# Kernel optimization log

Measured on AMD Instinct MI355X. Metric: run time of the kernel, lower is better.

## Reference

```python
import jax, jax.numpy as jnp
import numpy as np

N_NODES = 100000
N_EDGES = 600000
HIDDEN = 128


def setup_inputs() -> dict:
    key = jax.random.key(0)
    k_x, k_s, k_r, k_ws, k_wm = jax.random.split(key, 5)
    scale = 1.0 / np.sqrt(HIDDEN)
    return {
        "x": jax.random.normal(k_x, (N_NODES, HIDDEN), dtype=jnp.float32),
        "senders": jax.random.randint(k_s, (N_EDGES,), 0, N_NODES, dtype=jnp.int32),
        "receivers": jax.random.randint(k_r, (N_EDGES,), 0, N_NODES, dtype=jnp.int32),
        "weight_self": jax.random.normal(k_ws, (HIDDEN, HIDDEN), dtype=jnp.float32) * scale,
        "weight_msg": jax.random.normal(k_wm, (HIDDEN, HIDDEN), dtype=jnp.float32) * scale,
        "bias": jnp.zeros((HIDDEN,), dtype=jnp.float32),
    }


def reference(x, senders, receivers, weight_self, weight_msg, bias):
    n_nodes = x.shape[0]
    # gather messages along edges: (E, H)
    messages = x[senders]
    # scatter-add aggregate at receivers: (N, H)
    agg = jnp.zeros_like(x).at[receivers].add(messages)
    # in-degree count, clamped to >= 1
    degree = jnp.zeros((n_nodes,), dtype=x.dtype).at[receivers].add(1.0)
    degree = jnp.maximum(degree, 1.0)[:, None]
    msg_mean = agg / degree
    out = x @ weight_self + msg_mean @ weight_msg + bias
    return jax.nn.relu(out)
```

## Files before the change

kernel.cpp:

```cpp
#include <hip/hip_runtime.h>

#define N_NODES 100000
#define N_EDGES 600000
#define H 128
#define CAP 32

#define NB_FILL 586
#define NB_PREP 16
#define NB_CONV4 3125
#define NB_TOTAL (NB_FILL * 6 + (NB_PREP + NB_CONV4 - NB_FILL * 5))

#define BLK_NODES 64
#define N_BLKS ((N_NODES + BLK_NODES - 1) / BLK_NODES)

typedef short v8s __attribute__((ext_vector_type(8)));
typedef float v4f __attribute__((ext_vector_type(4)));

__device__ __forceinline__ unsigned short f2bf(float f) {
    unsigned int u = __float_as_uint(f);
    u = (u + 0x7fffu + ((u >> 16) & 1u)) >> 16;
    return (unsigned short)u;
}
__device__ __forceinline__ unsigned int pack2bf(float a, float b) {
    return (unsigned int)f2bf(a) | ((unsigned int)f2bf(b) << 16);
}
__device__ __forceinline__ void accum8(float* a, uint4 u) {
    a[0] += __uint_as_float(u.x << 16);
    a[1] += __uint_as_float(u.x & 0xffff0000u);
    a[2] += __uint_as_float(u.y << 16);
    a[3] += __uint_as_float(u.y & 0xffff0000u);
    a[4] += __uint_as_float(u.z << 16);
    a[5] += __uint_as_float(u.z & 0xffff0000u);
    a[6] += __uint_as_float(u.w << 16);
    a[7] += __uint_as_float(u.w & 0xffff0000u);
}

__global__ __launch_bounds__(256) void prep_fused_kernel(
    const float* __restrict__ x, unsigned int* __restrict__ xb4,
    const float* __restrict__ Ws, const float* __restrict__ Wm,
    unsigned short* __restrict__ Bperm,
    const int* __restrict__ senders, const int* __restrict__ receivers,
    int* __restrict__ cnt, int* __restrict__ slots)
{
    int b = blockIdx.x;
    bool isfill = (b % 6 == 0) && (b / 6 < NB_FILL);
    if (isfill) {
        int e = (b / 6) * 1024 + threadIdx.x;
#pragma unroll
        for (int k = 0; k < 4; ++k, e += 256) {
            if (e < N_EDGES) {
                int r = receivers[e];
                int s = senders[e];
                int pos = atomicAdd(&cnt[r], 1);
                if (pos < CAP) __builtin_nontemporal_store(s, &slots[r * CAP + pos]);
            }
        }
    } else {
        int o = (b < NB_FILL * 6) ? (b - b / 6 - 1) : (b - NB_FILL);
        if (o < NB_PREP) {
            int t = o * 256 + threadIdx.x;
            int kstep = t >> 9;
            int ntile = (t >> 6) & 7;
            int lane  = t & 63;
            int q = lane >> 4;
            int n = ntile * 16 + (lane & 15);
#pragma unroll
            for (int j = 0; j < 8; ++j) {
                int k = kstep * 32 + q * 8 + j;
                float v = (k < H) ? Ws[k * H + n] : Wm[(k - H) * H + n];
                Bperm[(size_t)t * 8 + j] = f2bf(v);
            }
        } else {
            int base = (o - NB_PREP) * 1024 + threadIdx.x;
#pragma unroll
            for (int k = 0; k < 4; ++k) {
                int i = base + k * 256;
                float4 v = ((const float4*)x)[i];
                uint2 ov;
                ov.x = pack2bf(v.x, v.y);
                ov.y = pack2bf(v.z, v.w);
                ((uint2*)xb4)[i] = ov;
            }
        }
    }
}

__global__ __launch_bounds__(256) void gather_gemm_kernel(
    const unsigned short* __restrict__ xb,
    const int* __restrict__ cnt,
    const int* __restrict__ slots,
    const unsigned short* __restrict__ Bperm,
    const float* __restrict__ bias,
    float* __restrict__ out)
{
    __shared__ unsigned short tile[2][16][65][8];

    const int t = threadIdx.x;
    const int w = t >> 6;
    const int lane = t & 63;
    const int node_base = blockIdx.x * BLK_NODES;
    const int sub = (lane >> 4) & 3;
    const int li  = lane & 15;

    for (int g = 0; g < 4; ++g) {
        int nl = w * 16 + g * 4 + sub;
        int node = node_base + nl;
        float a[8];
#pragma unroll
        for (int i = 0; i < 8; ++i) a[i] = 0.f;
        int d_true = 0;
        uint4 xcopy = make_uint4(0, 0, 0, 0);
        if (node < N_NODES) {
            xcopy = *(const uint4*)(xb + (size_t)node * H + li * 8);
            d_true = cnt[node];
            int d = d_true < CAP ? d_true : CAP;
            const int* sl = slots + node * CAP;
            int e = 0;
            for (; e + 3 < d; e += 4) {
                int i0 = sl[e];
                int i1 = sl[e + 1];
                int i2 = sl[e + 2];
                int i3 = sl[e + 3];
                uint4 u0 = *(const uint4*)(xb + (size_t)i0 * H + li * 8);
                uint4 u1 = *(const uint4*)(xb + (size_t)i1 * H + li * 8);
                uint4 u2 = *(const uint4*)(xb + (size_t)i2 * H + li * 8);
                uint4 u3 = *(const uint4*)(xb + (size_t)i3 * H + li * 8);
                accum8(a, u0);
                accum8(a, u1);
                accum8(a, u2);
                accum8(a, u3);
            }
            for (; e < d; ++e) {
                uint4 u0 = *(const uint4*)(xb + (size_t)sl[e] * H + li * 8);
                accum8(a, u0);
            }
        }
        float inv = 1.0f / fmaxf((float)d_true, 1.0f);
        uint4 o;
        o.x = pack2bf(a[0] * inv, a[1] * inv);
        o.y = pack2bf(a[2] * inv, a[3] * inv);
        o.z = pack2bf(a[4] * inv, a[5] * inv);
        o.w = pack2bf(a[6] * inv, a[7] * inv);
        *(uint4*)&tile[0][li][nl][0] = xcopy;
        *(uint4*)&tile[1][li][nl][0] = o;
    }
    __syncthreads();

    const int q  = lane >> 4;
    const int mr = lane & 15;

    v4f acc[4][2];
#pragma unroll
    for (int j = 0; j < 2; ++j) {
        float bv = bias[(2 * w + j) * 16 + mr];
#pragma unroll
        for (int s = 0; s < 4; ++s) acc[s][j] = (v4f){bv, bv, bv, bv};
    }

    const v8s* bp = (const v8s*)Bperm;
#pragma unroll
    for (int ks = 0; ks < 8; ++ks) {
        int buf = ks >> 2;
        int lic = (ks & 3) * 4 + q;
        v8s a[4];
#pragma unroll
        for (int s = 0; s < 4; ++s)
            a[s] = *(const v8s*)&tile[buf][lic][s * 16 + mr][0];
#pragma unroll
        for (int j = 0; j < 2; ++j) {
            v8s bfrag = bp[(ks * 8 + 2 * w + j) * 64 + lane];
#pragma unroll
            for (int s = 0; s < 4; ++s)
                acc[s][j] = __builtin_amdgcn_mfma_f32_16x16x32_bf16(a[s], bfrag, acc[s][j], 0, 0, 0);
        }
    }

#pragma unroll
    for (int s = 0; s < 4; ++s) {
#pragma unroll
        for (int r = 0; r < 4; ++r) {
            int row = node_base + s * 16 + q * 4 + r;
            if (row < N_NODES) {
#pragma unroll
                for (int j = 0; j < 2; ++j)
                    out[(size_t)row * H + (2 * w + j) * 16 + mr] = fmaxf(acc[s][j][r], 0.f);
            }
        }
    }
}

extern "C" void kernel_launch(void* const* d_in, const int* in_sizes, int n_in,
                              void* d_out, int out_size, void* d_ws, size_t ws_size,
                              hipStream_t stream) {
    const float* x        = (const float*)d_in[0];
    const int*   senders  = (const int*)d_in[1];
    const int*   receivers= (const int*)d_in[2];
    const float* Ws       = (const float*)d_in[3];
    const float* Wm       = (const float*)d_in[4];
    const float* bias     = (const float*)d_in[5];
    float*       out      = (float*)d_out;

    char* p = (char*)d_ws;
    unsigned short* xb    = (unsigned short*)p; p += (size_t)N_NODES * H * sizeof(unsigned short);
    unsigned short* Bperm = (unsigned short*)p; p += (size_t)256 * H * sizeof(unsigned short);
    int* cnt   = (int*)p; p += (size_t)N_NODES * sizeof(int);
    int* slots = (int*)p; p += (size_t)N_NODES * CAP * sizeof(int);

    hipMemsetAsync(cnt, 0, (size_t)N_NODES * sizeof(int), stream);

    prep_fused_kernel<<<NB_TOTAL, 256, 0, stream>>>(
        x, (unsigned int*)xb, Ws, Wm, Bperm, senders, receivers, cnt, slots);
    gather_gemm_kernel<<<N_BLKS, 256, 0, stream>>>(xb, cnt, slots, Bperm, bias, out);
}
```

Baseline: 186.2 us.

## Use 512-thread gather-GEMM blocks and vectorize edge and slot index loads

Result: faster. 178.3 us (-4.2%).

```diff
diff --git a/kernel.cpp b/kernel.cpp
--- a/kernel.cpp
+++ b/kernel.cpp
@@ -45,15 +45,18 @@
     int b = blockIdx.x;
     bool isfill = (b % 6 == 0) && (b / 6 < NB_FILL);
     if (isfill) {
-        int e = (b / 6) * 1024 + threadIdx.x;
-#pragma unroll
-        for (int k = 0; k < 4; ++k, e += 256) {
-            if (e < N_EDGES) {
-                int r = receivers[e];
-                int s = senders[e];
-                int pos = atomicAdd(&cnt[r], 1);
-                if (pos < CAP) __builtin_nontemporal_store(s, &slots[r * CAP + pos]);
-            }
+        int tid = (b / 6) * 256 + threadIdx.x;
+        if (tid < N_EDGES / 4) {
+            int4 r4 = ((const int4*)receivers)[tid];
+            int4 s4 = ((const int4*)senders)[tid];
+            int p0 = atomicAdd(&cnt[r4.x], 1);
+            int p1 = atomicAdd(&cnt[r4.y], 1);
+            int p2 = atomicAdd(&cnt[r4.z], 1);
+            int p3 = atomicAdd(&cnt[r4.w], 1);
+            if (p0 < CAP) __builtin_nontemporal_store(s4.x, &slots[r4.x * CAP + p0]);
+            if (p1 < CAP) __builtin_nontemporal_store(s4.y, &slots[r4.y * CAP + p1]);
+            if (p2 < CAP) __builtin_nontemporal_store(s4.z, &slots[r4.z * CAP + p2]);
+            if (p3 < CAP) __builtin_nontemporal_store(s4.w, &slots[r4.w * CAP + p3]);
         }
     } else {
         int o = (b < NB_FILL * 6) ? (b - b / 6 - 1) : (b - NB_FILL);
@@ -85,7 +88,7 @@
     }
 }
 
-__global__ __launch_bounds__(256) void gather_gemm_kernel(
+__global__ __launch_bounds__(512) void gather_gemm_kernel(
     const unsigned short* __restrict__ xb,
     const int* __restrict__ cnt,
     const int* __restrict__ slots,
@@ -102,8 +105,8 @@
     const int sub = (lane >> 4) & 3;
     const int li  = lane & 15;
 
-    for (int g = 0; g < 4; ++g) {
-        int nl = w * 16 + g * 4 + sub;
+    for (int g = 0; g < 2; ++g) {
+        int nl = w * 8 + g * 4 + sub;
         int node = node_base + nl;
         float a[8];
 #pragma unroll
@@ -117,14 +120,11 @@
             const int* sl = slots + node * CAP;
             int e = 0;
             for (; e + 3 < d; e += 4) {
-                int i0 = sl[e];
-                int i1 = sl[e + 1];
-                int i2 = sl[e + 2];
-                int i3 = sl[e + 3];
-                uint4 u0 = *(const uint4*)(xb + (size_t)i0 * H + li * 8);
-                uint4 u1 = *(const uint4*)(xb + (size_t)i1 * H + li * 8);
-                uint4 u2 = *(const uint4*)(xb + (size_t)i2 * H + li * 8);
-                uint4 u3 = *(const uint4*)(xb + (size_t)i3 * H + li * 8);
+                int4 i4 = *(const int4*)&sl[e];
+                uint4 u0 = *(const uint4*)(xb + (size_t)i4.x * H + li * 8);
+                uint4 u1 = *(const uint4*)(xb + (size_t)i4.y * H + li * 8);
+                uint4 u2 = *(const uint4*)(xb + (size_t)i4.z * H + li * 8);
+                uint4 u3 = *(const uint4*)(xb + (size_t)i4.w * H + li * 8);
                 accum8(a, u0);
                 accum8(a, u1);
                 accum8(a, u2);
@@ -149,12 +149,11 @@
     const int q  = lane >> 4;
     const int mr = lane & 15;
 
-    v4f acc[4][2];
-#pragma unroll
-    for (int j = 0; j < 2; ++j) {
-        float bv = bias[(2 * w + j) * 16 + mr];
-#pragma unroll
-        for (int s = 0; s < 4; ++s) acc[s][j] = (v4f){bv, bv, bv, bv};
+    v4f acc[4];
+    {
+        float bv = bias[w * 16 + mr];
+#pragma unroll
+        for (int s = 0; s < 4; ++s) acc[s] = (v4f){bv, bv, bv, bv};
     }
 
     const v8s* bp = (const v8s*)Bperm;
@@ -166,13 +165,10 @@
 #pragma unroll
         for (int s = 0; s < 4; ++s)
             a[s] = *(const v8s*)&tile[buf][lic][s * 16 + mr][0];
-#pragma unroll
-        for (int j = 0; j < 2; ++j) {
-            v8s bfrag = bp[(ks * 8 + 2 * w + j) * 64 + lane];
-#pragma unroll
-            for (int s = 0; s < 4; ++s)
-                acc[s][j] = __builtin_amdgcn_mfma_f32_16x16x32_bf16(a[s], bfrag, acc[s][j], 0, 0, 0);
-        }
+        v8s bfrag = bp[(ks * 8 + w) * 64 + lane];
+#pragma unroll
+        for (int s = 0; s < 4; ++s)
+            acc[s] = __builtin_amdgcn_mfma_f32_16x16x32_bf16(a[s], bfrag, acc[s], 0, 0, 0);
     }
 
 #pragma unroll
@@ -180,11 +176,8 @@
 #pragma unroll
         for (int r = 0; r < 4; ++r) {
             int row = node_base + s * 16 + q * 4 + r;
-            if (row < N_NODES) {
-#pragma unroll
-                for (int j = 0; j < 2; ++j)
-                    out[(size_t)row * H + (2 * w + j) * 16 + mr] = fmaxf(acc[s][j][r], 0.f);
-            }
+            if (row < N_NODES)
+                out[(size_t)row * H + w * 16 + mr] = fmaxf(acc[s][r], 0.f);
         }
     }
 }
@@ -210,5 +203,5 @@
 
     prep_fused_kernel<<<NB_TOTAL, 256, 0, stream>>>(
         x, (unsigned int*)xb, Ws, Wm, Bperm, senders, receivers, cnt, slots);
-    gather_gemm_kernel<<<N_BLKS, 256, 0, stream>>>(xb, cnt, slots, Bperm, bias, out);
-}
+    gather_gemm_kernel<<<N_BLKS, 512, 0, stream>>>(xb, cnt, slots, Bperm, bias, out);
+}
```
